# Performance work log

Hardware: AMD Instinct MI355X
Metric: run time of the kernel (lower is better)

Reference implementation:

```python
import jax, jax.numpy as jnp
import numpy as np

D = 256; HD = 16; G = 16; L = 2; HOP = 2; HK = 4
N = 16384; E = 49152; B = 256
VA = 128; VB = 8
SQRT2PI = float(np.sqrt(2.0 * 3.14159))  # module uses pi=3.14159


def group_norm(x, g=G, eps=1e-5):
    # torch GroupNorm(affine=False) on [N, D, 1]: normalize over each group of D//g channels
    n, d = x.shape
    xg = x.reshape(n, g, d // g)
    m = xg.mean(-1, keepdims=True)
    v = ((xg - m) ** 2).mean(-1, keepdims=True)
    return ((xg - m) * jax.lax.rsqrt(v + eps)).reshape(n, d)


def glin(x, w):
    # grouped 1x1 conv (no bias): x [n, g*din], w [g, dout, din] -> [n, g*dout]
    g, dout, din = w.shape
    return jnp.einsum('ngd,god->ngo', x.reshape(-1, g, din), w).reshape(-1, g * dout)


def multi_embed(idx, tables):
    # OGB-style encoder: sum of per-feature embeddings. idx [M,F], tables [F,V,D]
    out = tables[0][idx[:, 0]]
    for f in range(1, tables.shape[0]):
        out = out + tables[f][idx[:, f]]
    return out


def glb(x, pre_w, pre_b, gate_w, val_w, post_w, post_b):
    # GatedLinearBlock (dropout is identity in eval)
    xx = group_norm(x @ pre_w.T + pre_b)
    xx = jax.nn.relu(glin(xx, gate_w)) * glin(xx, val_w)
    return xx @ post_w.T + post_b


def glb2(xg, xv, gate_w, val_w, post_w, post_b):
    # GatedLinearBlock2: separate gate/value inputs, GroupNorm first
    gg = jax.nn.relu(glin(group_norm(xg), gate_w))
    vv = glin(group_norm(xv), val_w)
    return (gg * vv) @ post_w.T + post_b


def forward_impl(x_feat, edge_index, edge_attr, batch, batch_size,
                 edge_distance, atom_emb, bond2d_emb, gauss_means, gauss_stds,
                 attn_w, attn_b, scale_both,
                 conv_bond_emb, conv_pre_w, conv_gate_w, conv_val_w, conv_post_w, conv_post_b, conv_scale,
                 virt_pre_w, virt_pre_b, virt_gate_w, virt_val_w, virt_post_w, virt_post_b, virt_scale,
                 att_pre_w, att_pre_b, att_q_w, att_k_w, att_v_w, att_post_w, att_post_b, att_scale,
                 main_pre_w, main_pre_b, main_gate_w, main_val_w, main_post_w, main_post_b):
    src, dst = edge_index[0], edge_index[1]
    n = x_feat.shape[0]
    deg = jnp.clip(jax.ops.segment_sum(jnp.ones_like(dst), dst, num_segments=n) - 1, 0, 3)
    # --- edge features, mode='both': fuse 2D bond embedding with 3D gaussian features ---
    h2d = multi_embed(edge_attr, bond2d_emb)                      # [E, D]
    std = jnp.abs(gauss_stds) + 0.01
    diff = (edge_distance[:, None] - gauss_means[None, :]) / std
    h3d = jnp.exp(-0.5 * diff * diff) / (SQRT2PI * std)          # [E, D]
    w = jax.nn.sigmoid(jnp.concatenate([h2d, h3d], axis=-1) @ attn_w + attn_b[0])[:, None]
    h_e = w * h2d + (1.0 - w) * h3d
    h_in = jnp.exp(scale_both)[deg] * jax.ops.segment_sum(h_e, dst, num_segments=n)
    h_in = multi_embed(x_feat, atom_emb) + h_in                   # [N, D]
    h_virt = jnp.zeros((batch_size, D), h_in.dtype)
    h_att = jnp.zeros((batch_size, 2 * D // HD, HD, HD), h_in.dtype)
    for l in range(L):
        # --- ConvMessage: hop*kernel gated message-passing sublayers ---
        x_raw, x_out = h_in, jnp.zeros_like(h_in)
        for k in range(HK):
            if k > 0 and k % HOP == 0:
                x_raw, x_out = h_in + x_out, jnp.zeros_like(h_in)
            bond = multi_embed(edge_attr, conv_bond_emb[l, k])
            xp = x_raw @ conv_pre_w[l, k].T
            msg = glb2(xp[dst] + bond, xp[src] + bond,
                       conv_gate_w[l, k], conv_val_w[l, k], conv_post_w[l, k], conv_post_b[l, k])
            x_raw = jax.ops.segment_sum(msg, dst, num_segments=n)
            x_out = x_out + jnp.exp(conv_scale[l, k])[deg] * x_raw
        h_out = h_in + x_out
        # --- VirtMessage: graph-level virtual node with residual state ---
        h_virt = jax.ops.segment_sum(h_in, batch, num_segments=batch_size) + h_virt
        h_out = h_out + (jnp.exp(virt_scale[l]) * glb(h_virt, virt_pre_w[l], virt_pre_b[l],
                          virt_gate_w[l], virt_val_w[l], virt_post_w[l], virt_post_b[l]))[batch]
        # --- AttMessage: linear attention with per-graph scatter normalization ---
        xv0 = group_norm(h_in @ att_pre_w[l].T + att_pre_b[l])
        xq = jnp.exp(glin(xv0, att_q_w[l]) / np.sqrt(HD)).reshape(n, -1, HD)   # [N,32,16]
        xk = jnp.exp(glin(xv0, att_k_w[l]) / np.sqrt(HD)).reshape(n, -1, HD)
        xv = glin(xv0, att_v_w[l]).reshape(n, -1, HD)
        xkv = jnp.einsum('bnh,bnv->bnhv', xk, xv)                               # [N,32,16,16]
        h_att = jax.ops.segment_sum(xkv, batch, num_segments=batch_size) + h_att
        xk_sum = jax.ops.segment_sum(xk, batch, num_segments=batch_size)[batch]
        xq = xq / jnp.einsum('bnh,bnh->bn', xq, xk_sum)[:, :, None]
        att_out = jnp.einsum('bnh,bnhv->bnv', xq, h_att[batch]).reshape(n, 2 * D)
        h_out = h_out + jnp.exp(att_scale[l]) * (att_out @ att_post_w[l].T + att_post_b[l])
        # --- main gated block ---
        h_in = glb(h_out, main_pre_w[l], main_pre_b[l],
                   main_gate_w[l], main_val_w[l], main_post_w[l], main_post_b[l])
    return h_in


def setup_inputs() -> dict:
    key = jax.random.key(0)
    ks = iter(jax.random.split(key, 80))
    def rn(shape, s=0.05):
        return jax.random.normal(next(ks), shape, dtype=jnp.float32) * s
    inp = {}
    inp['x_feat'] = jax.random.randint(next(ks), (N, 9), 0, VA)
    inp['edge_index'] = jax.random.randint(next(ks), (2, E), 0, N)
    inp['edge_attr'] = jax.random.randint(next(ks), (E, 3), 0, VB)
    inp['batch'] = jnp.sort(jax.random.randint(next(ks), (N,), 0, B))
    inp['batch_size'] = B
    inp['edge_distance'] = jax.random.uniform(next(ks), (E,), dtype=jnp.float32) * 4.0
    inp['atom_emb'] = rn((9, VA, D))
    inp['bond2d_emb'] = rn((3, VB, D))
    inp['gauss_means'] = jax.random.uniform(next(ks), (D,), minval=2.0, maxval=3.0)
    inp['gauss_stds'] = jax.random.uniform(next(ks), (D,), minval=1.0, maxval=1.5)
    inp['attn_w'] = rn((2 * D,))
    inp['attn_b'] = rn((1,))
    inp['scale_both'] = jnp.full((4, D), np.log(0.1), jnp.float32)
    inp['conv_bond_emb'] = rn((L, HK, 3, VB, D))
    inp['conv_pre_w'] = rn((L, HK, D, D))
    inp['conv_gate_w'] = rn((L, HK, G, HD, HD))
    inp['conv_val_w'] = rn((L, HK, G, HD, HD))
    inp['conv_post_w'] = rn((L, HK, D, D))
    inp['conv_post_b'] = rn((L, HK, D))
    inp['conv_scale'] = jnp.full((L, HK, 4, D), np.log(0.1), jnp.float32)
    inp['virt_pre_w'] = rn((L, D, D)); inp['virt_pre_b'] = rn((L, D))
    inp['virt_gate_w'] = rn((L, G, 2 * HD, HD)); inp['virt_val_w'] = rn((L, G, 2 * HD, HD))
    inp['virt_post_w'] = rn((L, D, 2 * D)); inp['virt_post_b'] = rn((L, D))
    inp['virt_scale'] = jnp.full((L, D), np.log(0.01), jnp.float32)
    inp['att_pre_w'] = rn((L, D, D)); inp['att_pre_b'] = rn((L, D))
    inp['att_q_w'] = rn((L, G, 2 * HD, HD)); inp['att_k_w'] = rn((L, G, 2 * HD, HD)); inp['att_v_w'] = rn((L, G, 2 * HD, HD))
    inp['att_post_w'] = rn((L, D, 2 * D)); inp['att_post_b'] = rn((L, D))
    inp['att_scale'] = jnp.full((L, D), np.log(0.01), jnp.float32)
    inp['main_pre_w'] = rn((L, D, D)); inp['main_pre_b'] = rn((L, D))
    inp['main_gate_w'] = rn((L, G, 3 * HD, HD)); inp['main_val_w'] = rn((L, G, 3 * HD, HD))
    inp['main_post_w'] = rn((L, D, 3 * D)); inp['main_post_b'] = rn((L, D))
    return inp


def reference(x_feat, edge_index, edge_attr, batch, batch_size, edge_distance,
              atom_emb, bond2d_emb, gauss_means, gauss_stds, attn_w, attn_b, scale_both,
              conv_bond_emb, conv_pre_w, conv_gate_w, conv_val_w, conv_post_w, conv_post_b, conv_scale,
              virt_pre_w, virt_pre_b, virt_gate_w, virt_val_w, virt_post_w, virt_post_b, virt_scale,
              att_pre_w, att_pre_b, att_q_w, att_k_w, att_v_w, att_post_w, att_post_b, att_scale,
              main_pre_w, main_pre_b, main_gate_w, main_val_w, main_post_w, main_post_b):
    return forward_impl(x_feat, edge_index, edge_attr, batch, batch_size,
                        edge_distance, atom_emb, bond2d_emb, gauss_means, gauss_stds,
                        attn_w, attn_b, scale_both,
                        conv_bond_emb, conv_pre_w, conv_gate_w, conv_val_w, conv_post_w, conv_post_b, conv_scale,
                        virt_pre_w, virt_pre_b, virt_gate_w, virt_val_w, virt_post_w, virt_post_b, virt_scale,
                        att_pre_w, att_pre_b, att_q_w, att_k_w, att_v_w, att_post_w, att_post_b, att_scale,
                        main_pre_w, main_pre_b, main_gate_w, main_val_w, main_post_w, main_post_b)
```

## Files before the change

kernel.cpp:

```cpp
#include <hip/hip_runtime.h>
#include <cstdint>
#include <cstddef>
#include <type_traits>

#define NN 16384
#define EE 49152
#define BB 256

typedef _Float16 f16;
typedef _Float16 half8 __attribute__((ext_vector_type(8)));
typedef _Float16 half4v __attribute__((ext_vector_type(4)));
typedef _Float16 half2v __attribute__((ext_vector_type(2)));
typedef float floatx4 __attribute__((ext_vector_type(4)));

#if defined(__has_builtin)
#if __has_builtin(__builtin_amdgcn_fdot2)
#define HAVE_FDOT2 1
#endif
#endif

static constexpr size_t ND = (size_t)NN * 256;


__global__ __launch_bounds__(256) void count_deg_kernel(const int* __restrict__ dst, int* __restrict__ cnt, int e) {
// ... 50 lines not shown
    int* __restrict__ dst_s, float* __restrict__ ed_s) {
  int j = blockIdx.x * 256 + threadIdx.x;
  if (j >= EE) return;
  int e = elist[j];
  ea_s[j * 3 + 0] = eattr[e * 3 + 0];
  ea_s[j * 3 + 1] = eattr[e * 3 + 1];
  ea_s[j * 3 + 2] = eattr[e * 3 + 2];
  src_s[j] = src[e];
  dst_s[j] = dst[e];
  ed_s[j] = edist[e];
}
__global__ __launch_bounds__(256) void add3_kernel(float* __restrict__ dst,
    const float* __restrict__ a, const float* __restrict__ b, int n4) {
  int i = blockIdx.x * 256 + threadIdx.x;
  if (i >= n4) return;
  float4 x = reinterpret_cast<const float4*>(a)[i];
  float4 y = reinterpret_cast<const float4*>(b)[i];
  x.x += y.x; x.y += y.y; x.z += y.z; x.w += y.w;
  reinterpret_cast<float4*>(dst)[i] = x;
}
__global__ __launch_bounds__(256) void add3_both_kernel(float* __restrict__ dst, f16* __restrict__ dstH,
    const float* __restrict__ a, const float* __restrict__ b, int n4) {
  int i = blockIdx.x * 256 + threadIdx.x;
  if (i >= n4) return;
  float4 x = reinterpret_cast<const float4*>(a)[i];
  float4 y = reinterpret_cast<const float4*>(b)[i];
  x.x += y.x; x.y += y.y; x.z += y.z; x.w += y.w;
  reinterpret_cast<float4*>(dst)[i] = x;
  half4v h;
  h[0] = (f16)x.x; h[1] = (f16)x.y; h[2] = (f16)x.z; h[3] = (f16)x.w;
  reinterpret_cast<half4v*>(dstH)[i] = h;
}
__global__ __launch_bounds__(256) void bcast_add_kernel(float* __restrict__ ho,
    const float* __restrict__ vo, const float* __restrict__ vs, const int* __restrict__ batch) {
  int i4 = blockIdx.x * 256 + threadIdx.x;
  int i = i4 * 4;
  int n = i >> 8, c = i & 255;
  float4 h = reinterpret_cast<const float4*>(&ho[i])[0];
  float4 v = *reinterpret_cast<const float4*>(&vo[(size_t)batch[n] * 256 + c]);
  float4 s = *reinterpret_cast<const float4*>(&vs[c]);
  h.x += expf(s.x) * v.x; h.y += expf(s.y) * v.y;
  h.z += expf(s.z) * v.z; h.w += expf(s.w) * v.w;
  *reinterpret_cast<float4*>(&ho[i]) = h;
}
__global__ __launch_bounds__(256) void f2h_kernel(const float* __restrict__ in, f16* __restrict__ out, int n4) {
  int i = blockIdx.x * 256 + threadIdx.x;
  if (i >= n4) return;
  float4 v = reinterpret_cast<const float4*>(in)[i];
  half4v o;
  o[0] = (f16)v.x; o[1] = (f16)v.y; o[2] = (f16)v.z; o[3] = (f16)v.w;
  reinterpret_cast<half4v*>(out)[i] = o;
}

template <typename OUT>
__global__ __launch_bounds__(256) void seg_reduce_kernel(const f16* __restrict__ msg,
    const int* __restrict__ off, OUT* __restrict__ out) {
  int idx = blockIdx.x * 256 + threadIdx.x;
  int n = idx >> 6, c0 = (idx & 63) * 4;
  int j0 = off[n], j1 = off[n + 1];
  float a0 = 0.f, a1 = 0.f, a2 = 0.f, a3 = 0.f;
  int j = j0;
  for (; j + 1 < j1; j += 2) {
    half4v m0 = *reinterpret_cast<const half4v*>(&msg[(size_t)j * 256 + c0]);
    half4v m1 = *reinterpret_cast<const half4v*>(&msg[(size_t)(j + 1) * 256 + c0]);
    a0 += (float)m0[0] + (float)m1[0];
    a1 += (float)m0[1] + (float)m1[1];
    a2 += (float)m0[2] + (float)m1[2];
    a3 += (float)m0[3] + (float)m1[3];
  }
  if (j < j1) {
    half4v m0 = *reinterpret_cast<const half4v*>(&msg[(size_t)j * 256 + c0]);
    a0 += (float)m0[0]; a1 += (float)m0[1]; a2 += (float)m0[2]; a3 += (float)m0[3];
  }
  if constexpr (std::is_same<OUT, float>::value) {
    float4 o = {a0, a1, a2, a3};
    *reinterpret_cast<float4*>(&out[(size_t)n * 256 + c0]) = o;
  } else {
    half4v o;
    o[0] = (f16)a0; o[1] = (f16)a1; o[2] = (f16)a2; o[3] = (f16)a3;
    *reinterpret_cast<half4v*>(&out[(size_t)n * 256 + c0]) = o;
  }
}


__global__ __launch_bounds__(256) void edge_feat_kernel(
    const int* __restrict__ ea_s, const float* __restrict__ ed_s,
    const float* __restrict__ bond2d, const float* __restrict__ gmeans,
    const float* __restrict__ gstds, const float* __restrict__ attn_w,
    const float* __restrict__ attn_b, f16* __restrict__ msg) {
  int lane = threadIdx.x & 63;
  int j = blockIdx.x * 4 + (threadIdx.x >> 6);
  if (j >= EE) return;
  int a0 = ea_s[j * 3 + 0], a1 = ea_s[j * 3 + 1], a2 = ea_s[j * 3 + 2];
  float dist = ed_s[j];
  const float SQ2PI = sqrtf(2.0f * 3.14159f);
  int c0 = lane * 4;
  float4 b0 = *reinterpret_cast<const float4*>(&bond2d[a0 * 256 + c0]);
  float4 b1 = *reinterpret_cast<const float4*>(&bond2d[2048 + a1 * 256 + c0]);
  float4 b2 = *reinterpret_cast<const float4*>(&bond2d[4096 + a2 * 256 + c0]);
  float4 gm = *reinterpret_cast<const float4*>(&gmeans[c0]);
  float4 gs = *reinterpret_cast<const float4*>(&gstds[c0]);
  float4 w2 = *reinterpret_cast<const float4*>(&attn_w[c0]);
  float4 w3 = *reinterpret_cast<const float4*>(&attn_w[256 + c0]);
  float h2[4], h3[4];
  float part = 0.f;
#pragma unroll
  for (int i = 0; i < 4; i++) {
    h2[i] = (&b0.x)[i] + (&b1.x)[i] + (&b2.x)[i];
    float sd = fabsf((&gs.x)[i]) + 0.01f;
    float df = (dist - (&gm.x)[i]) / sd;
    h3[i] = expf(-0.5f * df * df) / (SQ2PI * sd);
    part += (&w2.x)[i] * h2[i] + (&w3.x)[i] * h3[i];
  }
#pragma unroll
  for (int off = 32; off > 0; off >>= 1) part += __shfl_xor(part, off);
  float wg = 1.f / (1.f + expf(-(part + attn_b[0])));
  half4v o;
#pragma unroll
  for (int i = 0; i < 4; i++) o[i] = (f16)(wg * h2[i] + (1.f - wg) * h3[i]);
  *reinterpret_cast<half4v*>(&msg[(size_t)j * 256 + c0]) = o;
}

__global__ __launch_bounds__(256) void atom_finish_kernel(
    const int* __restrict__ xf, const float* __restrict__ emb,
    const float* __restrict__ scale_both, const int* __restrict__ deg,
    const float* __restrict__ tmp, float* __restrict__ h_in, f16* __restrict__ h_inH) {
  int idx = blockIdx.x * 256 + threadIdx.x;
  int n = idx >> 6, c = (idx & 63) * 4;
  float a0 = 0.f, a1 = 0.f, a2 = 0.f, a3 = 0.f;
#pragma unroll
  for (int f = 0; f < 9; f++) {
    int v = xf[n * 9 + f];
    float4 e = *reinterpret_cast<const float4*>(&emb[((size_t)(f * 128 + v)) * 256 + c]);
    a0 += e.x; a1 += e.y; a2 += e.z; a3 += e.w;
  }
  int dg = deg[n];
  float4 s = *reinterpret_cast<const float4*>(&scale_both[dg * 256 + c]);
  float4 t = *reinterpret_cast<const float4*>(&tmp[(size_t)n * 256 + c]);
  float4 r;
  r.x = a0 + expf(s.x) * t.x; r.y = a1 + expf(s.y) * t.y;
  r.z = a2 + expf(s.z) * t.z; r.w = a3 + expf(s.w) * t.w;
  *reinterpret_cast<float4*>(&h_in[(size_t)n * 256 + c]) = r;
  half4v h;
  h[0] = (f16)r.x; h[1] = (f16)r.y; h[2] = (f16)r.z; h[3] = (f16)r.w;
  *reinterpret_cast<half4v*>(&h_inH[(size_t)n * 256 + c]) = h;
}

template <int MODE>
__global__ __launch_bounds__(256) void hgemm_kernel(
    const f16* __restrict__ A, const f16* __restrict__ W,
    const float* __restrict__ bias, const float* __restrict__ scale,
    const int* __restrict__ cnt, const int* __restrict__ deg,
    float* __restrict__ C, float* __restrict__ Cadd, f16* __restrict__ Cf, int K) {
  __shared__ f16 Ah[128 * 40];
  __shared__ f16 Wh[64 * 40];
  const int tid = threadIdx.x;
  const int row0 = blockIdx.x * 128, col0 = blockIdx.y * 64;
  const int lane = tid & 63;
  const int wave = tid >> 6;
  const int wr = (wave >> 1) * 64, wc = (wave & 1) * 32;
  const floatx4 fz = {0.f, 0.f, 0.f, 0.f};
  floatx4 acc[4][2];
#pragma unroll
  for (int m = 0; m < 4; m++)
#pragma unroll
    for (int n = 0; n < 2; n++) acc[m][n] = fz;
  const int q0 = tid * 2;
  const int rA0 = q0 >> 2, pA0 = q0 & 3;
  const int rA1 = (q0 + 1) >> 2, pA1 = (q0 + 1) & 3;
  const int rW = tid >> 2, pW = tid & 3;
  const int kb = (lane >> 4) * 8;
  const int fr = lane & 15;
  uint4 a0 = *reinterpret_cast<const uint4*>(&A[(size_t)(row0 + rA0) * K + pA0 * 8]);
  uint4 a1 = *reinterpret_cast<const uint4*>(&A[(size_t)(row0 + rA1) * K + pA1 * 8]);
  uint4 w0 = *reinterpret_cast<const uint4*>(&W[(size_t)(col0 + rW) * K + pW * 8]);
  for (int k0 = 0;;) {
    *reinterpret_cast<uint4*>(&Ah[rA0 * 40 + pA0 * 8]) = a0;
    *reinterpret_cast<uint4*>(&Ah[rA1 * 40 + pA1 * 8]) = a1;
    *reinterpret_cast<uint4*>(&Wh[rW * 40 + pW * 8]) = w0;
    __syncthreads();
    int kn = k0 + 32;
    if (kn < K) {
      a0 = *reinterpret_cast<const uint4*>(&A[(size_t)(row0 + rA0) * K + kn + pA0 * 8]);
      a1 = *reinterpret_cast<const uint4*>(&A[(size_t)(row0 + rA1) * K + kn + pA1 * 8]);
      w0 = *reinterpret_cast<const uint4*>(&W[(size_t)(col0 + rW) * K + kn + pW * 8]);
    }
    half8 af[4], wf[2];
#pragma unroll
    for (int m = 0; m < 4; m++)
      af[m] = *reinterpret_cast<const half8*>(&Ah[(wr + m * 16 + fr) * 40 + kb]);
#pragma unroll
    for (int n = 0; n < 2; n++)
      wf[n] = *reinterpret_cast<const half8*>(&Wh[(wc + n * 16 + fr) * 40 + kb]);
#pragma unroll
    for (int m = 0; m < 4; m++)
#pragma unroll
      for (int n = 0; n < 2; n++)
        acc[m][n] = __builtin_amdgcn_mfma_f32_16x16x32_f16(af[m], wf[n], acc[m][n], 0, 0, 0);
    if (kn >= K) break;
    __syncthreads();
    k0 = kn;
  }
  const int rl4 = (lane >> 4) * 4, cl = lane & 15;
#pragma unroll
  for (int m = 0; m < 4; m++) {
#pragma unroll
    for (int i = 0; i < 4; i++) {
      int row = row0 + wr + m * 16 + rl4 + i;
      float cb = (MODE >= 4) ? (float)cnt[row] : 1.f;
      int dg = (MODE >= 4) ? deg[row] : 0;
#pragma unroll
      for (int n = 0; n < 2; n++) {
        int col = col0 + wc + n * 16 + cl;
        float v = acc[m][n][i];
        size_t oi = (size_t)row * 256 + col;
        if (MODE >= 4) {
          v += cb * bias[col];
          float sc = expf(scale[dg * 256 + col]);
          if (MODE == 4) Cadd[oi] += sc * v;
          else Cadd[oi] = sc * v;
          if (Cf) Cf[oi] = (f16)v;
        } else if (MODE == 2) {
          v += bias[col];
          float nv = Cadd[oi] + expf(scale[col]) * v;
          if (C) C[oi] = nv;
          if (Cf) Cf[oi] = (f16)nv;
        } else {
          if (bias) v += bias[col];
          if (C) C[oi] = v;
          if (Cf) Cf[oi] = (f16)v;
        }
      }
    }
  }
}

__global__ __launch_bounds__(256) void conv_edge_kernel(
    const f16* __restrict__ xp, const int* __restrict__ ea_s,
    const int* __restrict__ src_s, const int* __restrict__ dst_s,
    const float* __restrict__ bond_emb, const float* __restrict__ gate_w,
    const float* __restrict__ val_w, f16* __restrict__ msg) {
  constexpr int RS = 264;
  __shared__ f16 sg[16 * RS];
  __shared__ f16 sv[16 * RS];
  int tid = threadIdx.x;
  for (int i = tid; i < 4096; i += 256) {
    int g = i >> 8, rem = i & 255;
    sg[g * RS + rem] = (f16)gate_w[i];
    sv[g * RS + rem] = (f16)val_w[i];
  }
  __syncthreads();
  int idx = blockIdx.x * 256 + tid;
  int j = idx >> 4, g = idx & 15;
  int a0 = ea_s[j * 3 + 0], a1 = ea_s[j * 3 + 1], a2 = ea_s[j * 3 + 2];
  int d = dst_s[j], s = src_s[j];
  half8 xd0 = *reinterpret_cast<const half8*>(&xp[(size_t)d * 256 + g * 16]);
  half8 xd1 = *reinterpret_cast<const half8*>(&xp[(size_t)d * 256 + g * 16 + 8]);
  half8 xs0 = *reinterpret_cast<const half8*>(&xp[(size_t)s * 256 + g * 16]);
  half8 xs1 = *reinterpret_cast<const half8*>(&xp[(size_t)s * 256 + g * 16 + 8]);
  const float4* b0p = reinterpret_cast<const float4*>(&bond_emb[a0 * 256 + g * 16]);
  const float4* b1p = reinterpret_cast<const float4*>(&bond_emb[2048 + a1 * 256 + g * 16]);
  const float4* b2p = reinterpret_cast<const float4*>(&bond_emb[4096 + a2 * 256 + g * 16]);
  float xg[16], xv[16];
  float mg = 0.f, mv = 0.f;
#pragma unroll
  for (int q = 0; q < 4; q++) {
    float4 b0 = b0p[q], b1 = b1p[q], b2 = b2p[q];
#pragma unroll
    for (int t = 0; t < 4; t++) {
      int i = q * 4 + t;
      float bo = (&b0.x)[t] + (&b1.x)[t] + (&b2.x)[t];
      float xd = (i < 8) ? (float)xd0[i & 7] : (float)xd1[i & 7];
      float xs = (i < 8) ? (float)xs0[i & 7] : (float)xs1[i & 7];
      xg[i] = xd + bo;
      xv[i] = xs + bo;
      mg += xg[i];
      mv += xv[i];
    }
  }
// ... 90 lines not shown
  }
  m *= (1.f / 16.f);
  float v = 0.f;
#pragma unroll
  for (int i = 0; i < 16; i++) {
    float d_ = x[i] - m;
    v += d_ * d_;
  }
  float r = rsqrtf(v * (1.f / 16.f) + 1e-5f);
#pragma unroll
  for (int i = 0; i < 16; i++) x[i] = (x[i] - m) * r;
#ifdef HAVE_FDOT2
  half2v xh[8];
#pragma unroll
  for (int q = 0; q < 8; q++) { xh[q][0] = (f16)x[2 * q]; xh[q][1] = (f16)x[2 * q + 1]; }
#endif
  const f16* gRow = &sg[g * RS];
  const f16* vRow = &sv[g * RS];
  f16 res[DOUT];
#pragma unroll
  for (int o = 0; o < DOUT; o++) {
    half8 gA = *reinterpret_cast<const half8*>(&gRow[o * 16]);
    half8 gB = *reinterpret_cast<const half8*>(&gRow[o * 16 + 8]);
    half8 vA = *reinterpret_cast<const half8*>(&vRow[o * 16]);
    half8 vB = *reinterpret_cast<const half8*>(&vRow[o * 16 + 8]);
    float ag = 0.f, av = 0.f;
#ifdef HAVE_FDOT2
#pragma unroll
    for (int q = 0; q < 4; q++) {
      half2v gq = {gA[2 * q], gA[2 * q + 1]};
      half2v g2 = {gB[2 * q], gB[2 * q + 1]};
      half2v vq = {vA[2 * q], vA[2 * q + 1]};
      half2v v2 = {vB[2 * q], vB[2 * q + 1]};
      ag = __builtin_amdgcn_fdot2(xh[q], gq, ag, false);
      ag = __builtin_amdgcn_fdot2(xh[q + 4], g2, ag, false);
      av = __builtin_amdgcn_fdot2(xh[q], vq, av, false);
      av = __builtin_amdgcn_fdot2(xh[q + 4], v2, av, false);
    }
#else
#pragma unroll
    for (int i = 0; i < 8; i++) {
      ag += x[i] * (float)gA[i] + x[i + 8] * (float)gB[i];
      av += x[i] * (float)vA[i] + x[i + 8] * (float)vB[i];
    }
#endif
    res[o] = (f16)(fmaxf(ag, 0.f) * av);
  }
  f16* op = &out[(size_t)n * (16 * DOUT) + g * DOUT];
#pragma unroll
  for (int q = 0; q < DOUT / 8; q++)
    *reinterpret_cast<half8*>(&op[q * 8]) = *reinterpret_cast<const half8*>(&res[q * 8]);
}

__global__ __launch_bounds__(256) void gn_vec_kernel(float* __restrict__ X) {
  int idx = blockIdx.x * 256 + threadIdx.x;
  int n = idx >> 6, q = idx & 63;
  float4 x = *reinterpret_cast<const float4*>(&X[(size_t)n * 256 + q * 4]);
  float s = x.x + x.y + x.z + x.w;
  float s2 = x.x * x.x + x.y * x.y + x.z * x.z + x.w * x.w;
  s += __shfl_xor(s, 1); s2 += __shfl_xor(s2, 1);
  s += __shfl_xor(s, 2); s2 += __shfl_xor(s2, 2);
  float m = s * (1.f / 16.f);
  float var = s2 * (1.f / 16.f) - m * m;
  float r = rsqrtf(var + 1e-5f);
  x.x = (x.x - m) * r; x.y = (x.y - m) * r;
  x.z = (x.z - m) * r; x.w = (x.w - m) * r;
  *reinterpret_cast<float4*>(&X[(size_t)n * 256 + q * 4]) = x;
}

template <bool FIRST>
__global__ __launch_bounds__(256) void att_graph_kernel(
    const float* __restrict__ xv0, const float* __restrict__ k_w,
    const float* __restrict__ v_w, const int* __restrict__ goff,
    float* __restrict__ h_att, float* __restrict__ xk_sum) {
  __shared__ float kx[8][256];
  __shared__ float vx[8][256];
  __shared__ float rows[8][256];
  const int tid = threadIdx.x;
  const int b = blockIdx.x >> 1, half = blockIdx.x & 1;
  const int p = half * 256 + tid;
  const int g = p >> 5;
  const int headLocal = tid >> 4;
  const int head = p >> 4, h = p & 15;
  float wk[16], wv[16];
#pragma unroll
  for (int i = 0; i < 4; i++) {
    float4 k0 = *reinterpret_cast<const float4*>(&k_w[p * 16 + i * 4]);
    float4 v0 = *reinterpret_cast<const float4*>(&v_w[p * 16 + i * 4]);
    wk[i * 4 + 0] = k0.x; wk[i * 4 + 1] = k0.y; wk[i * 4 + 2] = k0.z; wk[i * 4 + 3] = k0.w;
    wv[i * 4 + 0] = v0.x; wv[i * 4 + 1] = v0.y; wv[i * 4 + 2] = v0.z; wv[i * 4 + 3] = v0.w;
  }
  float hacc[16];
  if (FIRST) {
#pragma unroll
    for (int j = 0; j < 16; j++) hacc[j] = 0.f;
  } else {
    const float* hg = &h_att[(size_t)b * 8192];
#pragma unroll
    for (int j = 0; j < 16; j++) hacc[j] = hg[h * 512 + head * 16 + j];
  }
  float ks = 0.f;
  const int n0 = goff[b], n1 = goff[b + 1];
  float r[8];
#pragma unroll
  for (int nn = 0; nn < 8; nn++) {
    int n = n0 + nn;
    r[nn] = (n < n1) ? xv0[(size_t)n * 256 + tid] : 0.f;
  }
  for (int nbase = n0; nbase < n1; nbase += 8) {
#pragma unroll
    for (int nn = 0; nn < 8; nn++) rows[nn][tid] = r[nn];
    __syncthreads();
#pragma unroll
    for (int nn = 0; nn < 8; nn++) {
      int n = nbase + 8 + nn;
      r[nn] = (n < n1) ? xv0[(size_t)n * 256 + tid] : 0.f;
    }
#pragma unroll
    for (int nn = 0; nn < 8; nn++) {
      const float4* rp = reinterpret_cast<const float4*>(&rows[nn][g * 16]);
// ... 57 lines not shown
  int nl = tid >> 5, head = tid & 31;
  int g = head >> 1, j = head & 1;
  const float* ks = &xk_sum[(size_t)b * 512 + head * 16];
  for (int nbase = n0; nbase < n1; nbase += 8) {
    int n = nbase + nl;
    if (n >= n1) continue;
    float x[16];
    const float4* xp4 = reinterpret_cast<const float4*>(&xv0[(size_t)n * 256 + g * 16]);
#pragma unroll
    for (int q = 0; q < 4; q++) {
      float4 xq = xp4[q];
#pragma unroll
      for (int t = 0; t < 4; t++) x[q * 4 + t] = (&xq.x)[t];
    }
    float qv[16];
    float denom = 0.f;
#pragma unroll
    for (int h = 0; h < 16; h++) {
      const float4* wp = reinterpret_cast<const float4*>(&sqw[g * 260 + (j * 16 + h) * 16]);
      float a = 0.f;
#pragma unroll
      for (int q = 0; q < 4; q++) {
        float4 wq = wp[q];
#pragma unroll
        for (int t = 0; t < 4; t++) a += x[q * 4 + t] * (&wq.x)[t];
      }
      float e = expf(a * 0.25f);
      qv[h] = e;
      denom += e * ks[h];
    }
    float inv = 1.f / denom;
    float acc[16] = {0.f, 0.f, 0.f, 0.f, 0.f, 0.f, 0.f, 0.f,
                     0.f, 0.f, 0.f, 0.f, 0.f, 0.f, 0.f, 0.f};
#pragma unroll
    for (int h = 0; h < 16; h++) {
      float qh = qv[h];
      const float4* hp = reinterpret_cast<const float4*>(&hat[h * 644 + head * 20]);
#pragma unroll
      for (int q = 0; q < 4; q++) {
        float4 vq = hp[q];
        acc[q * 4 + 0] += qh * vq.x;
        acc[q * 4 + 1] += qh * vq.y;
        acc[q * 4 + 2] += qh * vq.z;
        acc[q * 4 + 3] += qh * vq.w;
      }
    }
    f16 res[16];
#pragma unroll
    for (int v = 0; v < 16; v++) res[v] = (f16)(acc[v] * inv);
    uint4* op = reinterpret_cast<uint4*>(&out[(size_t)n * 512 + head * 16]);
    op[0] = reinterpret_cast<const uint4*>(res)[0];
    op[1] = reinterpret_cast<const uint4*>(res)[1];
  }
}

__global__ __launch_bounds__(256) void virt_seg_kernel(const float* __restrict__ h_in,
    const int* __restrict__ goff, float* __restrict__ h_virt) {
  int b = blockIdx.x, c = threadIdx.x;
  float acc = h_virt[(size_t)b * 256 + c];
  int n0 = goff[b], n1 = goff[b + 1];
  for (int n = n0; n < n1; n++) acc += h_in[(size_t)n * 256 + c];
  h_virt[(size_t)b * 256 + c] = acc;
}


extern "C" void kernel_launch(void* const* d_in, const int* in_sizes, int n_in,
                              void* d_out, int out_size, void* d_ws, size_t ws_size,
                              hipStream_t stream) {
  const int* x_feat = (const int*)d_in[0];
  const int* eidx = (const int*)d_in[1];
  const int* eattr = (const int*)d_in[2];
  const int* batch = (const int*)d_in[3];
  const float* edist = (const float*)d_in[5];
  const float* atom_emb = (const float*)d_in[6];
  const float* bond2d = (const float*)d_in[7];
  const float* gmeans = (const float*)d_in[8];
  const float* gstds = (const float*)d_in[9];
  const float* attn_w = (const float*)d_in[10];
  const float* attn_b = (const float*)d_in[11];
  const float* scale_both = (const float*)d_in[12];
  const float* conv_bond_emb = (const float*)d_in[13];
  const float* conv_pre_w = (const float*)d_in[14];
  const float* conv_gate_w = (const float*)d_in[15];
  const float* conv_val_w = (const float*)d_in[16];
  const float* conv_post_w = (const float*)d_in[17];
  const float* conv_post_b = (const float*)d_in[18];
  const float* conv_scale = (const float*)d_in[19];
  const float* virt_pre_w = (const float*)d_in[20];
  const float* virt_pre_b = (const float*)d_in[21];
  const float* virt_gate_w = (const float*)d_in[22];
  const float* virt_val_w = (const float*)d_in[23];
  const float* virt_post_w = (const float*)d_in[24];
  const float* virt_post_b = (const float*)d_in[25];
  const float* virt_scale = (const float*)d_in[26];
  const float* att_pre_w = (const float*)d_in[27];
  const float* att_pre_b = (const float*)d_in[28];
  const float* att_q_w = (const float*)d_in[29];
  const float* att_k_w = (const float*)d_in[30];
  const float* att_v_w = (const float*)d_in[31];
  const float* att_post_w = (const float*)d_in[32];
  const float* att_post_b = (const float*)d_in[33];
  const float* att_scale = (const float*)d_in[34];
  const float* main_pre_w = (const float*)d_in[35];
  const float* main_pre_b = (const float*)d_in[36];
  const float* main_gate_w = (const float*)d_in[37];
  const float* main_val_w = (const float*)d_in[38];
  const float* main_post_w = (const float*)d_in[39];
  const float* main_post_b = (const float*)d_in[40];

  const int* src = eidx;
  const int* dst = eidx + EE;

  float* ws = (float*)d_ws;
  float* h_in = ws;
  float* h_out = ws + ND;
  float* x_raw = ws + 2 * ND;
  float* x_out = ws + 3 * ND;
  float* nodeA = ws + 4 * ND;
  f16* h_inH = (f16*)(ws + 5 * ND);
  f16* xrawH = (f16*)(ws + 5 * ND + ND / 2);
  f16* hTmp = (f16*)(ws + 6 * ND);
  f16* msgH = (f16*)(ws + 6 * ND + ND / 2);
  float* sm = ws + 8 * ND;
  f16* hW = (f16*)sm;
  float* h_virt = sm + 1179648;
  float* h_att = h_virt + 65536;
  float* xk_sum = h_att + 2097152;
  float* vt1 = xk_sum + 131072;
  float* vout = vt1 + 65536;
  f16* vmidH = (f16*)(vout + 65536);
  f16* virtH = vmidH + 131072;
  int* cnt = (int*)(virtH + 65536);
  int* deg = cnt + NN;
  int* goff = deg + NN;
  int* off = goff + BB + 1;
  int* cursor = off + NN + 1;
  int* elist = cursor + NN;
  int* ea_s = elist + EE;
  int* src_s = ea_s + 3 * EE;
  int* dst_s = src_s + EE;
  float* ed_s = (float*)(dst_s + EE);

  f16* wCpre = hW;
  f16* wCpost = hW + 524288;
  f16* wApre = hW + 1048576;
  f16* wApost = hW + 1179648;
  f16* wMpre = hW + 1441792;
  f16* wMpost = hW + 1572864;
  f16* wVpre = hW + 1966080;
  f16* wVpost = hW + 2097152;

  auto cvt = [&](const float* in, f16* out, int n) {
    f2h_kernel<<<n / 4 / 256, 256, 0, stream>>>(in, out, n / 4);
  };

  cvt(conv_pre_w, wCpre, 524288);
  cvt(conv_post_w, wCpost, 524288);
  cvt(att_pre_w, wApre, 131072);
  cvt(att_post_w, wApost, 262144);
  cvt(main_pre_w, wMpre, 131072);
  cvt(main_post_w, wMpost, 393216);
  cvt(virt_pre_w, wVpre, 131072);
  cvt(virt_post_w, wVpost, 262144);

  (void)hipMemsetAsync(cnt, 0, NN * sizeof(int), stream);
  count_deg_kernel<<<EE / 256, 256, 0, stream>>>(dst, cnt, EE);
  clip_deg_kernel<<<NN / 256, 256, 0, stream>>>(cnt, deg, NN);
  goff_kernel<<<(NN + 256) / 256, 256, 0, stream>>>(batch, goff, NN, BB);
  scan_off_kernel<<<1, 256, 0, stream>>>(cnt, off);
  copy_i_kernel<<<NN / 256, 256, 0, stream>>>(off, cursor, NN);
  fill_elist_kernel<<<EE / 256, 256, 0, stream>>>(dst, cursor, elist, EE);
  gather_edges_kernel<<<EE / 256, 256, 0, stream>>>(elist, eattr, src, dst, edist,
                                                    ea_s, src_s, dst_s, ed_s);

  edge_feat_kernel<<<EE / 4, 256, 0, stream>>>(ea_s, ed_s, bond2d, gmeans, gstds,
                                               attn_w, attn_b, msgH);
  seg_reduce_kernel<float><<<NN / 4, 256, 0, stream>>>(msgH, off, x_out);
  atom_finish_kernel<<<NN * 64 / 256, 256, 0, stream>>>(x_feat, atom_emb, scale_both, deg,
                                                        x_out, h_in, h_inH);
  (void)hipMemsetAsync(h_virt, 0, 65536 * 4, stream);

  const dim3 gN(NN / 128, 4), gB(BB / 128, 4);
  const int n4 = (int)(ND / 4);

  for (int l = 0; l < 2; l++) {
    const f16* curH = h_inH;
    for (int k = 0; k < 4; k++) {
      if (k == 2) {
        add3_both_kernel<<<n4 / 256, 256, 0, stream>>>(x_raw, xrawH, h_in, x_out, n4);
        curH = xrawH;
      }
      size_t lk = (size_t)(l * 4 + k);
      hgemm_kernel<0><<<gN, 256, 0, stream>>>(curH, wCpre + lk * 65536, nullptr, nullptr,
                                              nullptr, nullptr, nullptr, nullptr, hTmp, 256);
      conv_edge_kernel<<<EE * 16 / 256, 256, 0, stream>>>(
          hTmp, ea_s, src_s, dst_s, conv_bond_emb + lk * 6144,
          conv_gate_w + lk * 4096, conv_val_w + lk * 4096, msgH);
      seg_reduce_kernel<f16><<<NN / 4, 256, 0, stream>>>(msgH, off, hTmp);
      if (k == 0 || k == 2)
        hgemm_kernel<5><<<gN, 256, 0, stream>>>(hTmp, wCpost + lk * 65536,
                                                conv_post_b + lk * 256, conv_scale + lk * 1024,
                                                cnt, deg, nullptr, x_out, xrawH, 256);
      else
        hgemm_kernel<4><<<gN, 256, 0, stream>>>(hTmp, wCpost + lk * 65536,
                                                conv_post_b + lk * 256, conv_scale + lk * 1024,
                                                cnt, deg, nullptr, x_out, xrawH, 256);
      curH = xrawH;
    }
    add3_kernel<<<n4 / 256, 256, 0, stream>>>(h_out, h_in, x_out, n4);

    virt_seg_kernel<<<BB, 256, 0, stream>>>(h_in, goff, h_virt);
    cvt(h_virt, virtH, 65536);
    hgemm_kernel<0><<<gB, 256, 0, stream>>>(virtH, wVpre + (size_t)l * 65536,
                                            virt_pre_b + (size_t)l * 256, nullptr, nullptr,
                                            nullptr, vt1, nullptr, nullptr, 256);
    glb_mid_kernel<32><<<BB * 16 / 256, 256, 0, stream>>>(
        vt1, virt_gate_w + (size_t)l * 8192, virt_val_w + (size_t)l * 8192, vmidH);
    hgemm_kernel<0><<<gB, 256, 0, stream>>>(vmidH, wVpost + (size_t)l * 131072,
                                            virt_post_b + (size_t)l * 256, nullptr, nullptr,
                                            nullptr, vout, nullptr, nullptr, 512);
    bcast_add_kernel<<<n4 / 256, 256, 0, stream>>>(
        h_out, vout, virt_scale + (size_t)l * 256, batch);

    hgemm_kernel<0><<<gN, 256, 0, stream>>>(h_inH, wApre + (size_t)l * 65536,
                                            att_pre_b + (size_t)l * 256, nullptr, nullptr,
                                            nullptr, nodeA, nullptr, nullptr, 256);
    gn_vec_kernel<<<NN * 64 / 256, 256, 0, stream>>>(nodeA);
    if (l == 0)
      att_graph_kernel<true><<<BB * 2, 256, 0, stream>>>(
          nodeA, att_k_w + (size_t)l * 8192, att_v_w + (size_t)l * 8192, goff, h_att, xk_sum);
    else
      att_graph_kernel<false><<<BB * 2, 256, 0, stream>>>(
          nodeA, att_k_w + (size_t)l * 8192, att_v_w + (size_t)l * 8192, goff, h_att, xk_sum);
    att_out_kernel<<<BB, 256, 0, stream>>>(
        nodeA, att_q_w + (size_t)l * 8192, xk_sum, h_att, goff, msgH);
    hgemm_kernel<2><<<gN, 256, 0, stream>>>(msgH, wApost + (size_t)l * 131072,
                                            att_post_b + (size_t)l * 256,
                                            att_scale + (size_t)l * 256, nullptr, nullptr,
                                            nullptr, h_out, hTmp, 512);

    hgemm_kernel<0><<<gN, 256, 0, stream>>>(hTmp, wMpre + (size_t)l * 65536,
                                            main_pre_b + (size_t)l * 256, nullptr, nullptr,
                                            nullptr, nodeA, nullptr, nullptr, 256);
    glb_mid_kernel<48><<<NN * 16 / 256, 256, 0, stream>>>(
        nodeA, main_gate_w + (size_t)l * 12288, main_val_w + (size_t)l * 12288, msgH);
    float* hdst = (l == 1) ? (float*)d_out : h_in;
    f16* hdstH = (l == 1) ? nullptr : h_inH;
    hgemm_kernel<0><<<gN, 256, 0, stream>>>(msgH, wMpost + (size_t)l * 196608,
                                            main_post_b + (size_t)l * 256, nullptr, nullptr,
                                            nullptr, hdst, nullptr, hdstH, 768);
  }
}
```

Measured before the change: 1.054 ms.

## Fuse segment-sum reduction of edge messages into conv post GEMM A-tile loads

Removes the separate seg_reduce pass over edge messages inside each conv hop. The conv post GEMM now gathers and sums each node's incoming edge messages while loading its A tile, using the CSR offsets. This saves a kernel launch and the write and re-read of the reduced node tensor. In exchange, the GEMM loader runs irregular, variable-length loops, and each message row is read once per column block (gridDim.y times) rather than once overall, which can stall the MFMA pipeline.

```diff
diff --git a/kernel.cpp b/kernel.cpp
--- a/kernel.cpp
+++ b/kernel.cpp
@@ -126,34 +126,18 @@
   reinterpret_cast<half4v*>(out)[i] = o;
 }
 
-template <typename OUT>
-__global__ __launch_bounds__(256) void seg_reduce_kernel(const f16* __restrict__ msg,
-    const int* __restrict__ off, OUT* __restrict__ out) {
+__global__ __launch_bounds__(256) void seg_reduce_f_kernel(const f16* __restrict__ msg,
+    const int* __restrict__ off, float* __restrict__ out) {
   int idx = blockIdx.x * 256 + threadIdx.x;
   int n = idx >> 6, c0 = (idx & 63) * 4;
   int j0 = off[n], j1 = off[n + 1];
   float a0 = 0.f, a1 = 0.f, a2 = 0.f, a3 = 0.f;
-  int j = j0;
-  for (; j + 1 < j1; j += 2) {
-    half4v m0 = *reinterpret_cast<const half4v*>(&msg[(size_t)j * 256 + c0]);
-    half4v m1 = *reinterpret_cast<const half4v*>(&msg[(size_t)(j + 1) * 256 + c0]);
-    a0 += (float)m0[0] + (float)m1[0];
-    a1 += (float)m0[1] + (float)m1[1];
-    a2 += (float)m0[2] + (float)m1[2];
-    a3 += (float)m0[3] + (float)m1[3];
-  }
-  if (j < j1) {
+  for (int j = j0; j < j1; j++) {
     half4v m0 = *reinterpret_cast<const half4v*>(&msg[(size_t)j * 256 + c0]);
     a0 += (float)m0[0]; a1 += (float)m0[1]; a2 += (float)m0[2]; a3 += (float)m0[3];
   }
-  if constexpr (std::is_same<OUT, float>::value) {
-    float4 o = {a0, a1, a2, a3};
-    *reinterpret_cast<float4*>(&out[(size_t)n * 256 + c0]) = o;
-  } else {
-    half4v o;
-    o[0] = (f16)a0; o[1] = (f16)a1; o[2] = (f16)a2; o[3] = (f16)a3;
-    *reinterpret_cast<half4v*>(&out[(size_t)n * 256 + c0]) = o;
-  }
+  float4 o = {a0, a1, a2, a3};
+  *reinterpret_cast<float4*>(&out[(size_t)n * 256 + c0]) = o;
 }
 
 
@@ -220,11 +204,24 @@
   *reinterpret_cast<half4v*>(&h_inH[(size_t)n * 256 + c]) = h;
 }
 
-template <int MODE>
+__device__ __forceinline__ half8 seg_gather8(const f16* __restrict__ A, int j0, int j1, int col) {
+  float s[8] = {0.f, 0.f, 0.f, 0.f, 0.f, 0.f, 0.f, 0.f};
+  for (int j = j0; j < j1; j++) {
+    half8 m = *reinterpret_cast<const half8*>(&A[(size_t)j * 256 + col]);
+#pragma unroll
+    for (int t = 0; t < 8; t++) s[t] += (float)m[t];
+  }
+  half8 r;
+#pragma unroll
+  for (int t = 0; t < 8; t++) r[t] = (f16)s[t];
+  return r;
+}
+
+template <int MODE, bool SEG>
 __global__ __launch_bounds__(256) void hgemm_kernel(
     const f16* __restrict__ A, const f16* __restrict__ W,
     const float* __restrict__ bias, const float* __restrict__ scale,
-    const int* __restrict__ cnt, const int* __restrict__ deg,
+    const int* __restrict__ cnt, const int* __restrict__ deg, const int* __restrict__ off,
     float* __restrict__ C, float* __restrict__ Cadd, f16* __restrict__ Cf, int K) {
   __shared__ f16 Ah[128 * 40];
   __shared__ f16 Wh[64 * 40];
@@ -245,19 +242,35 @@
   const int rW = tid >> 2, pW = tid & 3;
   const int kb = (lane >> 4) * 8;
   const int fr = lane & 15;
-  uint4 a0 = *reinterpret_cast<const uint4*>(&A[(size_t)(row0 + rA0) * K + pA0 * 8]);
-  uint4 a1 = *reinterpret_cast<const uint4*>(&A[(size_t)(row0 + rA1) * K + pA1 * 8]);
-  uint4 w0 = *reinterpret_cast<const uint4*>(&W[(size_t)(col0 + rW) * K + pW * 8]);
+  int jA0s = 0, jA0e = 0, jA1s = 0, jA1e = 0;
+  if (SEG) {
+    jA0s = off[row0 + rA0]; jA0e = off[row0 + rA0 + 1];
+    jA1s = off[row0 + rA1]; jA1e = off[row0 + rA1 + 1];
+  }
+  half8 a0, a1, w0;
+  if (SEG) {
+    a0 = seg_gather8(A, jA0s, jA0e, pA0 * 8);
+    a1 = seg_gather8(A, jA1s, jA1e, pA1 * 8);
+  } else {
+    a0 = *reinterpret_cast<const half8*>(&A[(size_t)(row0 + rA0) * K + pA0 * 8]);
+    a1 = *reinterpret_cast<const half8*>(&A[(size_t)(row0 + rA1) * K + pA1 * 8]);
+  }
+  w0 = *reinterpret_cast<const half8*>(&W[(size_t)(col0 + rW) * K + pW * 8]);
   for (int k0 = 0;;) {
-    *reinterpret_cast<uint4*>(&Ah[rA0 * 40 + pA0 * 8]) = a0;
-    *reinterpret_cast<uint4*>(&Ah[rA1 * 40 + pA1 * 8]) = a1;
-    *reinterpret_cast<uint4*>(&Wh[rW * 40 + pW * 8]) = w0;
+    *reinterpret_cast<half8*>(&Ah[rA0 * 40 + pA0 * 8]) = a0;
+    *reinterpret_cast<half8*>(&Ah[rA1 * 40 + pA1 * 8]) = a1;
+    *reinterpret_cast<half8*>(&Wh[rW * 40 + pW * 8]) = w0;
     __syncthreads();
     int kn = k0 + 32;
     if (kn < K) {
-      a0 = *reinterpret_cast<const uint4*>(&A[(size_t)(row0 + rA0) * K + kn + pA0 * 8]);
-      a1 = *reinterpret_cast<const uint4*>(&A[(size_t)(row0 + rA1) * K + kn + pA1 * 8]);
-      w0 = *reinterpret_cast<const uint4*>(&W[(size_t)(col0 + rW) * K + kn + pW * 8]);
+      if (SEG) {
+        a0 = seg_gather8(A, jA0s, jA0e, kn + pA0 * 8);
+        a1 = seg_gather8(A, jA1s, jA1e, kn + pA1 * 8);
+      } else {
+        a0 = *reinterpret_cast<const half8*>(&A[(size_t)(row0 + rA0) * K + kn + pA0 * 8]);
+        a1 = *reinterpret_cast<const half8*>(&A[(size_t)(row0 + rA1) * K + kn + pA1 * 8]);
+      }
+      w0 = *reinterpret_cast<const half8*>(&W[(size_t)(col0 + rW) * K + kn + pW * 8]);
     }
     half8 af[4], wf[2];
 #pragma unroll
@@ -795,7 +808,7 @@
 
   edge_feat_kernel<<<EE / 4, 256, 0, stream>>>(ea_s, ed_s, bond2d, gmeans, gstds,
                                                attn_w, attn_b, msgH);
-  seg_reduce_kernel<float><<<NN / 4, 256, 0, stream>>>(msgH, off, x_out);
+  seg_reduce_f_kernel<<<NN / 4, 256, 0, stream>>>(msgH, off, x_out);
   atom_finish_kernel<<<NN * 64 / 256, 256, 0, stream>>>(x_feat, atom_emb, scale_both, deg,
                                                         x_out, h_in, h_inH);
   (void)hipMemsetAsync(h_virt, 0, 65536 * 4, stream);
@@ -811,40 +824,45 @@
         curH = xrawH;
       }
       size_t lk = (size_t)(l * 4 + k);
-      hgemm_kernel<0><<<gN, 256, 0, stream>>>(curH, wCpre + lk * 65536, nullptr, nullptr,
-                                              nullptr, nullptr, nullptr, nullptr, hTmp, 256);
+      hgemm_kernel<0, false><<<gN, 256, 0, stream>>>(curH, wCpre + lk * 65536, nullptr,
+                                                     nullptr, nullptr, nullptr, nullptr,
+                                                     nullptr, nullptr, hTmp, 256);
       conv_edge_kernel<<<EE * 16 / 256, 256, 0, stream>>>(
           hTmp, ea_s, src_s, dst_s, conv_bond_emb + lk * 6144,
           conv_gate_w + lk * 4096, conv_val_w + lk * 4096, msgH);
-      seg_reduce_kernel<f16><<<NN / 4, 256, 0, stream>>>(msgH, off, hTmp);
       if (k == 0 || k == 2)
-        hgemm_kernel<5><<<gN, 256, 0, stream>>>(hTmp, wCpost + lk * 65536,
-                                                conv_post_b + lk * 256, conv_scale + lk * 1024,
-                                                cnt, deg, nullptr, x_out, xrawH, 256);
+        hgemm_kernel<5, true><<<gN, 256, 0, stream>>>(msgH, wCpost + lk * 65536,
+                                                      conv_post_b + lk * 256,
+                                                      conv_scale + lk * 1024, cnt, deg, off,
+                                                      nullptr, x_out, xrawH, 256);
       else
-        hgemm_kernel<4><<<gN, 256, 0, stream>>>(hTmp, wCpost + lk * 65536,
-                                                conv_post_b + lk * 256, conv_scale + lk * 1024,
-                                                cnt, deg, nullptr, x_out, xrawH, 256);
+        hgemm_kernel<4, true><<<gN, 256, 0, stream>>>(msgH, wCpost + lk * 65536,
+                                                      conv_post_b + lk * 256,
+                                                      conv_scale + lk * 1024, cnt, deg, off,
+                                                      nullptr, x_out, xrawH, 256);
       curH = xrawH;
     }
     add3_kernel<<<n4 / 256, 256, 0, stream>>>(h_out, h_in, x_out, n4);
 
     virt_seg_kernel<<<BB, 256, 0, stream>>>(h_in, goff, h_virt);
     cvt(h_virt, virtH, 65536);
-    hgemm_kernel<0><<<gB, 256, 0, stream>>>(virtH, wVpre + (size_t)l * 65536,
-                                            virt_pre_b + (size_t)l * 256, nullptr, nullptr,
-                                            nullptr, vt1, nullptr, nullptr, 256);
+    hgemm_kernel<0, false><<<gB, 256, 0, stream>>>(virtH, wVpre + (size_t)l * 65536,
+                                                   virt_pre_b + (size_t)l * 256, nullptr,
+                                                   nullptr, nullptr, nullptr,
+                                                   vt1, nullptr, nullptr, 256);
     glb_mid_kernel<32><<<BB * 16 / 256, 256, 0, stream>>>(
         vt1, virt_gate_w + (size_t)l * 8192, virt_val_w + (size_t)l * 8192, vmidH);
-    hgemm_kernel<0><<<gB, 256, 0, stream>>>(vmidH, wVpost + (size_t)l * 131072,
-                                            virt_post_b + (size_t)l * 256, nullptr, nullptr,
-                                            nullptr, vout, nullptr, nullptr, 512);
+    hgemm_kernel<0, false><<<gB, 256, 0, stream>>>(vmidH, wVpost + (size_t)l * 131072,
+                                                   virt_post_b + (size_t)l * 256, nullptr,
+                                                   nullptr, nullptr, nullptr,
+                                                   vout, nullptr, nullptr, 512);
     bcast_add_kernel<<<n4 / 256, 256, 0, stream>>>(
         h_out, vout, virt_scale + (size_t)l * 256, batch);
 
-    hgemm_kernel<0><<<gN, 256, 0, stream>>>(h_inH, wApre + (size_t)l * 65536,
-                                            att_pre_b + (size_t)l * 256, nullptr, nullptr,
-                                            nullptr, nodeA, nullptr, nullptr, 256);
+    hgemm_kernel<0, false><<<gN, 256, 0, stream>>>(h_inH, wApre + (size_t)l * 65536,
+                                                   att_pre_b + (size_t)l * 256, nullptr,
+                                                   nullptr, nullptr, nullptr,
+                                                   nodeA, nullptr, nullptr, 256);
     gn_vec_kernel<<<NN * 64 / 256, 256, 0, stream>>>(nodeA);
     if (l == 0)
       att_graph_kernel<true><<<BB * 2, 256, 0, stream>>>(
@@ -854,20 +872,23 @@
           nodeA, att_k_w + (size_t)l * 8192, att_v_w + (size_t)l * 8192, goff, h_att, xk_sum);
     att_out_kernel<<<BB, 256, 0, stream>>>(
         nodeA, att_q_w + (size_t)l * 8192, xk_sum, h_att, goff, msgH);
-    hgemm_kernel<2><<<gN, 256, 0, stream>>>(msgH, wApost + (size_t)l * 131072,
-                                            att_post_b + (size_t)l * 256,
-                                            att_scale + (size_t)l * 256, nullptr, nullptr,
-                                            nullptr, h_out, hTmp, 512);
-
-    hgemm_kernel<0><<<gN, 256, 0, stream>>>(hTmp, wMpre + (size_t)l * 65536,
-                                            main_pre_b + (size_t)l * 256, nullptr, nullptr,
-                                            nullptr, nodeA, nullptr, nullptr, 256);
+    hgemm_kernel<2, false><<<gN, 256, 0, stream>>>(msgH, wApost + (size_t)l * 131072,
+                                                   att_post_b + (size_t)l * 256,
+                                                   att_scale + (size_t)l * 256, nullptr,
+                                                   nullptr, nullptr,
+                                                   nullptr, h_out, hTmp, 512);
+
+    hgemm_kernel<0, false><<<gN, 256, 0, stream>>>(hTmp, wMpre + (size_t)l * 65536,
+                                                   main_pre_b + (size_t)l * 256, nullptr,
+                                                   nullptr, nullptr, nullptr,
+                                                   nodeA, nullptr, nullptr, 256);
     glb_mid_kernel<48><<<NN * 16 / 256, 256, 0, stream>>>(
         nodeA, main_gate_w + (size_t)l * 12288, main_val_w + (size_t)l * 12288, msgH);
     float* hdst = (l == 1) ? (float*)d_out : h_in;
     f16* hdstH = (l == 1) ? nullptr : h_inH;
-    hgemm_kernel<0><<<gN, 256, 0, stream>>>(msgH, wMpost + (size_t)l * 196608,
-                                            main_post_b + (size_t)l * 256, nullptr, nullptr,
-                                            nullptr, hdst, nullptr, hdstH, 768);
-  }
-}
+    hgemm_kernel<0, false><<<gN, 256, 0, stream>>>(msgH, wMpost + (size_t)l * 196608,
+                                                   main_post_b + (size_t)l * 256, nullptr,
+                                                   nullptr, nullptr, nullptr,
+                                                   hdst, nullptr, hdstH, 768);
+  }
+}
```

Result: slower. 1.231 ms (+16.8%).

## Fuse virtual-node GLB into one kernel and fold GroupNorm into attention pre-GEMM

Applied to the files above, without the earlier changes.

The virtual-node path (segment sum, f16 conversion, pre GEMM, gated mid, post GEMM) is replaced by a single per-graph kernel that does the matvecs in fp32 from shared memory. This removes several small launches and the fp16 weight conversions. The attention pre-GEMM gains a MODE 6 epilogue that computes the 16-channel GroupNorm with lane shuffles, so the separate gn_vec pass over the node tensor is no longer needed. The fused virtual kernel reads full fp32 weights per block with scalar FMA, and the shuffle-based norm relies on the MFMA output layout placing each 16-column group across 16 adjacent lanes.

```diff
diff --git a/kernel.cpp b/kernel.cpp
--- a/kernel.cpp
+++ b/kernel.cpp
@@ -281,14 +281,14 @@
 #pragma unroll
     for (int i = 0; i < 4; i++) {
       int row = row0 + wr + m * 16 + rl4 + i;
-      float cb = (MODE >= 4) ? (float)cnt[row] : 1.f;
-      int dg = (MODE >= 4) ? deg[row] : 0;
+      float cb = (MODE == 4 || MODE == 5) ? (float)cnt[row] : 1.f;
+      int dg = (MODE == 4 || MODE == 5) ? deg[row] : 0;
 #pragma unroll
       for (int n = 0; n < 2; n++) {
         int col = col0 + wc + n * 16 + cl;
         float v = acc[m][n][i];
         size_t oi = (size_t)row * 256 + col;
-        if (MODE >= 4) {
+        if (MODE == 4 || MODE == 5) {
           v += cb * bias[col];
           float sc = expf(scale[dg * 256 + col]);
           if (MODE == 4) Cadd[oi] += sc * v;
@@ -299,6 +299,17 @@
           float nv = Cadd[oi] + expf(scale[col]) * v;
           if (C) C[oi] = nv;
           if (Cf) Cf[oi] = (f16)nv;
+        } else if (MODE == 6) {
+          v += bias[col];
+          float s1 = v, s2 = v * v;
+#pragma unroll
+          for (int o_ = 1; o_ < 16; o_ <<= 1) {
+            s1 += __shfl_xor(s1, o_);
+            s2 += __shfl_xor(s2, o_);
+          }
+          float mean = s1 * (1.f / 16.f);
+          float var = s2 * (1.f / 16.f) - mean * mean;
+          C[oi] = (v - mean) * rsqrtf(var + 1e-5f);
         } else {
           if (bias) v += bias[col];
           if (C) C[oi] = v;
@@ -495,20 +506,67 @@
     *reinterpret_cast<half8*>(&op[q * 8]) = *reinterpret_cast<const half8*>(&res[q * 8]);
 }
 
-__global__ __launch_bounds__(256) void gn_vec_kernel(float* __restrict__ X) {
-  int idx = blockIdx.x * 256 + threadIdx.x;
-  int n = idx >> 6, q = idx & 63;
-  float4 x = *reinterpret_cast<const float4*>(&X[(size_t)n * 256 + q * 4]);
-  float s = x.x + x.y + x.z + x.w;
-  float s2 = x.x * x.x + x.y * x.y + x.z * x.z + x.w * x.w;
-  s += __shfl_xor(s, 1); s2 += __shfl_xor(s2, 1);
-  s += __shfl_xor(s, 2); s2 += __shfl_xor(s2, 2);
-  float m = s * (1.f / 16.f);
-  float var = s2 * (1.f / 16.f) - m * m;
-  float r = rsqrtf(var + 1e-5f);
-  x.x = (x.x - m) * r; x.y = (x.y - m) * r;
-  x.z = (x.z - m) * r; x.w = (x.w - m) * r;
-  *reinterpret_cast<float4*>(&X[(size_t)n * 256 + q * 4]) = x;
+__global__ __launch_bounds__(256) void virt_fused_kernel(
+    const float* __restrict__ h_in, const int* __restrict__ goff,
+    const float* __restrict__ preW, const float* __restrict__ preb,
+    const float* __restrict__ gateW, const float* __restrict__ valW,
+    const float* __restrict__ postW, const float* __restrict__ postb,
+    float* __restrict__ h_virt, float* __restrict__ vout) {
+  __shared__ float sx[256];
+  __shared__ float xx[256];
+  __shared__ float vv[512];
+  int tid = threadIdx.x, b = blockIdx.x;
+  int n0 = goff[b], n1 = goff[b + 1];
+  float acc = h_virt[(size_t)b * 256 + tid];
+  for (int n = n0; n < n1; n++) acc += h_in[(size_t)n * 256 + tid];
+  h_virt[(size_t)b * 256 + tid] = acc;
+  sx[tid] = acc;
+  __syncthreads();
+  float dot = preb[tid];
+  const float4* wrow = reinterpret_cast<const float4*>(&preW[(size_t)tid * 256]);
+  const float4* sx4 = reinterpret_cast<const float4*>(sx);
+#pragma unroll 8
+  for (int q = 0; q < 64; q++) {
+    float4 w = wrow[q];
+    float4 s = sx4[q];
+    dot += w.x * s.x + w.y * s.y + w.z * s.z + w.w * s.w;
+  }
+  float s1 = dot, s2 = dot * dot;
+#pragma unroll
+  for (int o_ = 1; o_ < 16; o_ <<= 1) {
+    s1 += __shfl_xor(s1, o_);
+    s2 += __shfl_xor(s2, o_);
+  }
+  float mean = s1 * (1.f / 16.f);
+  float var = s2 * (1.f / 16.f) - mean * mean;
+  xx[tid] = (dot - mean) * rsqrtf(var + 1e-5f);
+  __syncthreads();
+#pragma unroll
+  for (int rep = 0; rep < 2; rep++) {
+    int o = tid + rep * 256;
+    int g = o >> 5, o2 = o & 31;
+    const float4* gw = reinterpret_cast<const float4*>(&gateW[(size_t)(g * 32 + o2) * 16]);
+    const float4* vw = reinterpret_cast<const float4*>(&valW[(size_t)(g * 32 + o2) * 16]);
+    const float4* xg4 = reinterpret_cast<const float4*>(&xx[g * 16]);
+    float ag = 0.f, av = 0.f;
+#pragma unroll
+    for (int q = 0; q < 4; q++) {
+      float4 wg = gw[q], wv = vw[q], xq = xg4[q];
+      ag += wg.x * xq.x + wg.y * xq.y + wg.z * xq.z + wg.w * xq.w;
+      av += wv.x * xq.x + wv.y * xq.y + wv.z * xq.z + wv.w * xq.w;
+    }
+    vv[o] = fmaxf(ag, 0.f) * av;
+  }
+  __syncthreads();
+  float outv = postb[tid];
+  const float4* prow = reinterpret_cast<const float4*>(&postW[(size_t)tid * 512]);
+  const float4* vv4 = reinterpret_cast<const float4*>(vv);
+#pragma unroll 8
+  for (int q = 0; q < 128; q++) {
+    float4 w = prow[q], s = vv4[q];
+    outv += w.x * s.x + w.y * s.y + w.z * s.z + w.w * s.w;
+  }
+  vout[(size_t)b * 256 + tid] = outv;
 }
 
 template <bool FIRST>
@@ -672,15 +730,6 @@
     op[0] = reinterpret_cast<const uint4*>(res)[0];
     op[1] = reinterpret_cast<const uint4*>(res)[1];
   }
-}
-
-__global__ __launch_bounds__(256) void virt_seg_kernel(const float* __restrict__ h_in,
-    const int* __restrict__ goff, float* __restrict__ h_virt) {
-  int b = blockIdx.x, c = threadIdx.x;
-  float acc = h_virt[(size_t)b * 256 + c];
-  int n0 = goff[b], n1 = goff[b + 1];
-  for (int n = n0; n < n1; n++) acc += h_in[(size_t)n * 256 + c];
-  h_virt[(size_t)b * 256 + c] = acc;
 }
 
 
@@ -746,11 +795,8 @@
   float* h_virt = sm + 1179648;
   float* h_att = h_virt + 65536;
   float* xk_sum = h_att + 2097152;
-  float* vt1 = xk_sum + 131072;
-  float* vout = vt1 + 65536;
-  f16* vmidH = (f16*)(vout + 65536);
-  f16* virtH = vmidH + 131072;
-  int* cnt = (int*)(virtH + 65536);
+  float* vout = xk_sum + 131072;
+  int* cnt = (int*)(vout + 65536);
   int* deg = cnt + NN;
   int* goff = deg + NN;
   int* off = goff + BB + 1;
@@ -767,8 +813,6 @@
   f16* wApost = hW + 1179648;
   f16* wMpre = hW + 1441792;
   f16* wMpost = hW + 1572864;
-  f16* wVpre = hW + 1966080;
-  f16* wVpost = hW + 2097152;
 
   auto cvt = [&](const float* in, f16* out, int n) {
     f2h_kernel<<<n / 4 / 256, 256, 0, stream>>>(in, out, n / 4);
@@ -780,8 +824,6 @@
   cvt(att_post_w, wApost, 262144);
   cvt(main_pre_w, wMpre, 131072);
   cvt(main_post_w, wMpost, 393216);
-  cvt(virt_pre_w, wVpre, 131072);
-  cvt(virt_post_w, wVpost, 262144);
 
   (void)hipMemsetAsync(cnt, 0, NN * sizeof(int), stream);
   count_deg_kernel<<<EE / 256, 256, 0, stream>>>(dst, cnt, EE);
@@ -800,7 +842,7 @@
                                                         x_out, h_in, h_inH);
   (void)hipMemsetAsync(h_virt, 0, 65536 * 4, stream);
 
-  const dim3 gN(NN / 128, 4), gB(BB / 128, 4);
+  const dim3 gN(NN / 128, 4);
   const int n4 = (int)(ND / 4);
 
   for (int l = 0; l < 2; l++) {
@@ -829,23 +871,16 @@
     }
     add3_kernel<<<n4 / 256, 256, 0, stream>>>(h_out, h_in, x_out, n4);
 
-    virt_seg_kernel<<<BB, 256, 0, stream>>>(h_in, goff, h_virt);
-    cvt(h_virt, virtH, 65536);
-    hgemm_kernel<0><<<gB, 256, 0, stream>>>(virtH, wVpre + (size_t)l * 65536,
-                                            virt_pre_b + (size_t)l * 256, nullptr, nullptr,
-                                            nullptr, vt1, nullptr, nullptr, 256);
-    glb_mid_kernel<32><<<BB * 16 / 256, 256, 0, stream>>>(
-        vt1, virt_gate_w + (size_t)l * 8192, virt_val_w + (size_t)l * 8192, vmidH);
-    hgemm_kernel<0><<<gB, 256, 0, stream>>>(vmidH, wVpost + (size_t)l * 131072,
-                                            virt_post_b + (size_t)l * 256, nullptr, nullptr,
-                                            nullptr, vout, nullptr, nullptr, 512);
+    virt_fused_kernel<<<BB, 256, 0, stream>>>(
+        h_in, goff, virt_pre_w + (size_t)l * 65536, virt_pre_b + (size_t)l * 256,
+        virt_gate_w + (size_t)l * 8192, virt_val_w + (size_t)l * 8192,
+        virt_post_w + (size_t)l * 131072, virt_post_b + (size_t)l * 256, h_virt, vout);
     bcast_add_kernel<<<n4 / 256, 256, 0, stream>>>(
         h_out, vout, virt_scale + (size_t)l * 256, batch);
 
-    hgemm_kernel<0><<<gN, 256, 0, stream>>>(h_inH, wApre + (size_t)l * 65536,
+    hgemm_kernel<6><<<gN, 256, 0, stream>>>(h_inH, wApre + (size_t)l * 65536,
                                             att_pre_b + (size_t)l * 256, nullptr, nullptr,
                                             nullptr, nodeA, nullptr, nullptr, 256);
-    gn_vec_kernel<<<NN * 64 / 256, 256, 0, stream>>>(nodeA);
     if (l == 0)
       att_graph_kernel<true><<<BB * 2, 256, 0, stream>>>(
           nodeA, att_k_w + (size_t)l * 8192, att_v_w + (size_t)l * 8192, goff, h_att, xk_sum);
```

After: 1.018 ms. 3.4% less time.
